# Kernel tuning notes

Measured on AMD Instinct MI355X. Metric: run time of the kernel, lower is better.

Reference implementation:

```python
import jax, jax.numpy as jnp
import numpy as np

TOTAL = 33554432  # 2**25 flat logits
NSEG = 65536      # number of jagged segments (avg len 512)


def setup_inputs() -> dict:
    key = jax.random.key(0)
    logits = jax.random.normal(key, (TOTAL,), dtype=jnp.float32)
    # Build a valid inclusive prefix-sum of segment lengths that ends exactly at TOTAL.
    rng = np.random.default_rng(0)
    raw = rng.integers(256, 769, size=NSEG).astype(np.float64)
    prefix = np.floor(np.cumsum(raw) / raw.sum() * TOTAL).astype(np.int64)
    prefix[-1] = TOTAL
    prefix_sum = jnp.asarray(prefix, dtype=jnp.int64)
    return {"logits": logits, "prefix_sum": prefix_sum}


def reference(logits, prefix_sum):
    # prefix_sum[j] = end index (exclusive) of segment j in the flat logits array.
    N = logits.shape[0]
    B = prefix_sum.shape[0]
    # segment id of element i = number of segment ends <= i
    seg = jnp.searchsorted(prefix_sum, jnp.arange(N, dtype=prefix_sum.dtype), side="right")
    # numerically stable per-segment log-softmax
    seg_max = jax.ops.segment_max(logits, seg, num_segments=B)
    seg_max = jnp.where(jnp.isfinite(seg_max), seg_max, jnp.zeros_like(seg_max))  # guard empty segments
    shifted = logits - seg_max[seg]
    seg_sum = jax.ops.segment_sum(jnp.exp(shifted), seg, num_segments=B)
    return shifted - jnp.log(seg_sum)[seg]
```

## Files before the change

### kernel.cpp

```cpp
#include <hip/hip_runtime.h>
#include <math.h>

#define WAVES_PER_BLOCK 4
#define THREADS (WAVES_PER_BLOCK * 64)
#define MAX_V4 3

__global__ __launch_bounds__(THREADS)
void jls_kernel(const float* __restrict__ logits,
                const int* __restrict__ prefix,
                float* __restrict__ out, int nseg) {
    const int wave = threadIdx.x >> 6;
    const int lane = threadIdx.x & 63;
    const int seg = blockIdx.x * WAVES_PER_BLOCK + wave;
    if (seg >= nseg) return;

    const int start = (seg == 0) ? 0 : prefix[seg - 1];
    const int end   = prefix[seg];
    const int len   = end - start;
    if (len <= 0) return;

    int a0 = (start + 3) & ~3;
    if (a0 > end) a0 = end;
    const int head = a0 - start;
    const int nv   = (end - a0) >> 2;
    const int tail_start = a0 + (nv << 2);
    const int tail = end - tail_start;

    float s = 0.f;

    if (nv <= 64 * MAX_V4) {
        float hv = 0.f, tv = 0.f;
        float4 v[MAX_V4];
        bool valid[MAX_V4];

        if (lane < head) { hv = logits[start + lane]; s += __expf(hv); }
        #pragma unroll
        for (int k = 0; k < MAX_V4; ++k) {
            const int vi = lane + k * 64;
            valid[k] = vi < nv;
            if (valid[k]) {
                v[k] = *reinterpret_cast<const float4*>(logits + a0 + (vi << 2));
                s += __expf(v[k].x) + __expf(v[k].y) + __expf(v[k].z) + __expf(v[k].w);
            }
        }
        if (lane < tail) { tv = logits[tail_start + lane]; s += __expf(tv); }

        #pragma unroll
        for (int off = 32; off > 0; off >>= 1)
            s += __shfl_xor(s, off, 64);
        const float lg = __logf(s);

        if (lane < head) out[start + lane] = hv - lg;
        #pragma unroll
        for (int k = 0; k < MAX_V4; ++k) {
            if (valid[k]) {
                const int vi = lane + k * 64;
                float4 r;
                r.x = v[k].x - lg; r.y = v[k].y - lg;
                r.z = v[k].z - lg; r.w = v[k].w - lg;
                *reinterpret_cast<float4*>(out + a0 + (vi << 2)) = r;
            }
        }
        if (lane < tail) out[tail_start + lane] = tv - lg;
    } else {
        for (int i = start + lane; i < end; i += 64)
            s += __expf(logits[i]);
        #pragma unroll
        for (int off = 32; off > 0; off >>= 1)
            s += __shfl_xor(s, off, 64);
        const float lg = __logf(s);
        for (int i = start + lane; i < end; i += 64)
            out[i] = logits[i] - lg;
    }
}

extern "C" void kernel_launch(void* const* d_in, const int* in_sizes, int n_in,
                              void* d_out, int out_size, void* d_ws, size_t ws_size,
                              hipStream_t stream) {
    const float* logits = (const float*)d_in[0];
    const int* prefix = (const int*)d_in[1];
    float* out = (float*)d_out;
    const int nseg = in_sizes[1];

    const int blocks = (nseg + WAVES_PER_BLOCK - 1) / WAVES_PER_BLOCK;
    jls_kernel<<<blocks, THREADS, 0, stream>>>(logits, prefix, out, nseg);
}
```

Baseline: 47.71 us.

## Process two segments per wave with batched loads and nontemporal stores

```diff
diff --git a/kernel.cpp b/kernel.cpp
--- a/kernel.cpp
+++ b/kernel.cpp
@@ -3,7 +3,24 @@
 
 #define WAVES_PER_BLOCK 4
 #define THREADS (WAVES_PER_BLOCK * 64)
+#define SEGS_PER_WAVE 2
 #define MAX_V4 3
+
+typedef float f32x4 __attribute__((ext_vector_type(4)));
+
+__device__ __forceinline__ void seg_generic(const float* __restrict__ logits,
+                                            float* __restrict__ out,
+                                            int start, int end, int lane) {
+    float s = 0.f;
+    for (int i = start + lane; i < end; i += 64)
+        s += __expf(logits[i]);
+    #pragma unroll
+    for (int off = 32; off > 0; off >>= 1)
+        s += __shfl_xor(s, off, 64);
+    const float lg = __logf(s);
+    for (int i = start + lane; i < end; i += 64)
+        out[i] = logits[i] - lg;
+}
 
 __global__ __launch_bounds__(THREADS)
 void jls_kernel(const float* __restrict__ logits,
@@ -11,66 +28,81 @@
                 float* __restrict__ out, int nseg) {
     const int wave = threadIdx.x >> 6;
     const int lane = threadIdx.x & 63;
-    const int seg = blockIdx.x * WAVES_PER_BLOCK + wave;
-    if (seg >= nseg) return;
+    const int seg0 = (blockIdx.x * WAVES_PER_BLOCK + wave) * SEGS_PER_WAVE;
+    if (seg0 >= nseg) return;
+    const bool has1 = (seg0 + 1) < nseg;
 
-    const int start = (seg == 0) ? 0 : prefix[seg - 1];
-    const int end   = prefix[seg];
-    const int len   = end - start;
-    if (len <= 0) return;
+    const int pA = (seg0 == 0) ? 0 : prefix[seg0 - 1];
+    const int pB = prefix[seg0];
+    const int pC = has1 ? prefix[seg0 + 1] : pB;
 
-    int a0 = (start + 3) & ~3;
-    if (a0 > end) a0 = end;
-    const int head = a0 - start;
-    const int nv   = (end - a0) >> 2;
-    const int tail_start = a0 + (nv << 2);
-    const int tail = end - tail_start;
+    int a0A = (pA + 3) & ~3; if (a0A > pB) a0A = pB;
+    const int headA = a0A - pA;
+    const int nvA   = (pB - a0A) >> 2;
+    const int tsA   = a0A + (nvA << 2);
+    const int tailA = pB - tsA;
 
-    float s = 0.f;
+    int a0B = (pB + 3) & ~3; if (a0B > pC) a0B = pC;
+    const int headB = a0B - pB;
+    const int nvB   = (pC - a0B) >> 2;
+    const int tsB   = a0B + (nvB << 2);
+    const int tailB = pC - tsB;
 
-    if (nv <= 64 * MAX_V4) {
-        float hv = 0.f, tv = 0.f;
-        float4 v[MAX_V4];
-        bool valid[MAX_V4];
+    if (nvA <= 64 * MAX_V4 && nvB <= 64 * MAX_V4) {
+        float hvA = 0.f, tvA = 0.f, hvB = 0.f, tvB = 0.f;
+        f32x4 vA[MAX_V4], vB[MAX_V4];
+        bool okA[MAX_V4], okB[MAX_V4];
 
-        if (lane < head) { hv = logits[start + lane]; s += __expf(hv); }
+        if (lane < headA) hvA = logits[pA + lane];
+        if (lane < headB) hvB = logits[pB + lane];
         #pragma unroll
         for (int k = 0; k < MAX_V4; ++k) {
             const int vi = lane + k * 64;
-            valid[k] = vi < nv;
-            if (valid[k]) {
-                v[k] = *reinterpret_cast<const float4*>(logits + a0 + (vi << 2));
-                s += __expf(v[k].x) + __expf(v[k].y) + __expf(v[k].z) + __expf(v[k].w);
+            okA[k] = vi < nvA;
+            if (okA[k]) vA[k] = *reinterpret_cast<const f32x4*>(logits + a0A + (vi << 2));
+            okB[k] = vi < nvB;
+            if (okB[k]) vB[k] = *reinterpret_cast<const f32x4*>(logits + a0B + (vi << 2));
+        }
+        if (lane < tailA) tvA = logits[tsA + lane];
+        if (lane < tailB) tvB = logits[tsB + lane];
+
+        float sA = (lane < headA) ? __expf(hvA) : 0.f;
+        float sB = (lane < headB) ? __expf(hvB) : 0.f;
+        #pragma unroll
+        for (int k = 0; k < MAX_V4; ++k) {
+            if (okA[k]) sA += __expf(vA[k].x) + __expf(vA[k].y) + __expf(vA[k].z) + __expf(vA[k].w);
+            if (okB[k]) sB += __expf(vB[k].x) + __expf(vB[k].y) + __expf(vB[k].z) + __expf(vB[k].w);
+        }
+        if (lane < tailA) sA += __expf(tvA);
+        if (lane < tailB) sB += __expf(tvB);
+
+        #pragma unroll
+        for (int off = 32; off > 0; off >>= 1) {
+            sA += __shfl_xor(sA, off, 64);
+            sB += __shfl_xor(sB, off, 64);
+        }
+        const float lgA = __logf(sA);
+        const float lgB = __logf(sB);
+
+        if (lane < headA) out[pA + lane] = hvA - lgA;
+        if (lane < headB) out[pB + lane] = hvB - lgB;
+        #pragma unroll
+        for (int k = 0; k < MAX_V4; ++k) {
+            const int vi = lane + k * 64;
+            if (okA[k]) {
+                f32x4 r = vA[k] - lgA;
+                __builtin_nontemporal_store(r, reinterpret_cast<f32x4*>(out + a0A + (vi << 2)));
+            }
+            if (okB[k]) {
+                f32x4 r = vB[k] - lgB;
+                __builtin_nontemporal_store(r, reinterpret_cast<f32x4*>(out + a0B + (vi << 2)));
             }
         }
-        if (lane < tail) { tv = logits[tail_start + lane]; s += __expf(tv); }
-
-        #pragma unroll
-        for (int off = 32; off > 0; off >>= 1)
-            s += __shfl_xor(s, off, 64);
-        const float lg = __logf(s);
-
-        if (lane < head) out[start + lane] = hv - lg;
-        #pragma unroll
-        for (int k = 0; k < MAX_V4; ++k) {
-            if (valid[k]) {
-                const int vi = lane + k * 64;
-                float4 r;
-                r.x = v[k].x - lg; r.y = v[k].y - lg;
-                r.z = v[k].z - lg; r.w = v[k].w - lg;
-                *reinterpret_cast<float4*>(out + a0 + (vi << 2)) = r;
-            }
-        }
-        if (lane < tail) out[tail_start + lane] = tv - lg;
+        if (lane < tailA) out[tsA + lane] = tvA - lgA;
+        if (lane < tailB) out[tsB + lane] = tvB - lgB;
     } else {
-        for (int i = start + lane; i < end; i += 64)
-            s += __expf(logits[i]);
-        #pragma unroll
-        for (int off = 32; off > 0; off >>= 1)
-            s += __shfl_xor(s, off, 64);
-        const float lg = __logf(s);
-        for (int i = start + lane; i < end; i += 64)
-            out[i] = logits[i] - lg;
+        seg_generic(logits, out, pA, pB, lane);
+        if (has1) seg_generic(logits, out, pB, pC, lane);
     }
 }
 
@@ -82,6 +114,7 @@
     float* out = (float*)d_out;
     const int nseg = in_sizes[1];
 
-    const int blocks = (nseg + WAVES_PER_BLOCK - 1) / WAVES_PER_BLOCK;
+    const int segs_per_block = WAVES_PER_BLOCK * SEGS_PER_WAVE;
+    const int blocks = (nseg + segs_per_block - 1) / segs_per_block;
     jls_kernel<<<blocks, THREADS, 0, stream>>>(logits, prefix, out, nseg);
 }
```

After: 48.25 us. No clear change (+1.1%).

## Use persistent waves with double-buffered segment prefetch and nontemporal stores

Applied to the files above, without the earlier changes.

```diff
diff --git a/kernel.cpp b/kernel.cpp
--- a/kernel.cpp
+++ b/kernel.cpp
@@ -1,9 +1,75 @@
 #include <hip/hip_runtime.h>
 #include <math.h>
 
-#define WAVES_PER_BLOCK 4
-#define THREADS (WAVES_PER_BLOCK * 64)
+#define WPB 4
+#define THREADS (WPB * 64)
 #define MAX_V4 3
+#define NBLOCKS 2048
+
+typedef float f32x4 __attribute__((ext_vector_type(4)));
+
+struct Seg {
+    int start, end, a0, nv, ts, head, tail;
+    float hv, tv;
+    f32x4 v0, v1, v2;
+};
+
+__device__ __forceinline__ void seg_generic(const float* __restrict__ logits,
+                                            float* __restrict__ out,
+                                            int start, int end, int lane) {
+    float s = 0.f;
+    for (int i = start + lane; i < end; i += 64)
+        s += __expf(logits[i]);
+    #pragma unroll
+    for (int off = 32; off > 0; off >>= 1)
+        s += __shfl_xor(s, off, 64);
+    const float lg = __logf(s);
+    for (int i = start + lane; i < end; i += 64)
+        out[i] = logits[i] - lg;
+}
+
+__device__ __forceinline__ void issue_data(Seg& S, int start, int end,
+                                           const float* __restrict__ logits, int lane) {
+    S.start = start; S.end = end;
+    int a0 = (start + 3) & ~3; if (a0 > end) a0 = end;
+    S.a0 = a0;
+    S.head = a0 - start;
+    const int nv = (end - a0) >> 2;
+    S.nv = nv;
+    S.ts = a0 + (nv << 2);
+    S.tail = end - S.ts;
+    S.hv = 0.f; S.tv = 0.f;
+    S.v0 = 0.f; S.v1 = 0.f; S.v2 = 0.f;
+    if (nv > 64 * MAX_V4) return;
+    if (lane < S.head) S.hv = logits[start + lane];
+    if (lane       < nv) S.v0 = *reinterpret_cast<const f32x4*>(logits + a0 + (lane << 2));
+    if (lane + 64  < nv) S.v1 = *reinterpret_cast<const f32x4*>(logits + a0 + ((lane + 64) << 2));
+    if (lane + 128 < nv) S.v2 = *reinterpret_cast<const f32x4*>(logits + a0 + ((lane + 128) << 2));
+    if (lane < S.tail) S.tv = logits[S.ts + lane];
+}
+
+__device__ __forceinline__ void finish(const Seg& S, const float* __restrict__ logits,
+                                       float* __restrict__ out, int lane) {
+    if (S.nv > 64 * MAX_V4) { seg_generic(logits, out, S.start, S.end, lane); return; }
+    const bool ok0 = lane < S.nv, ok1 = lane + 64 < S.nv, ok2 = lane + 128 < S.nv;
+    float s = (lane < S.head) ? __expf(S.hv) : 0.f;
+    if (ok0) s += __expf(S.v0.x) + __expf(S.v0.y) + __expf(S.v0.z) + __expf(S.v0.w);
+    if (ok1) s += __expf(S.v1.x) + __expf(S.v1.y) + __expf(S.v1.z) + __expf(S.v1.w);
+    if (ok2) s += __expf(S.v2.x) + __expf(S.v2.y) + __expf(S.v2.z) + __expf(S.v2.w);
+    if (lane < S.tail) s += __expf(S.tv);
+    #pragma unroll
+    for (int off = 32; off > 0; off >>= 1)
+        s += __shfl_xor(s, off, 64);
+    const float lg = __logf(s);
+    if (lane < S.head) out[S.start + lane] = S.hv - lg;
+    if (ok0) { f32x4 r = S.v0 - lg;
+        __builtin_nontemporal_store(r, reinterpret_cast<f32x4*>(out + S.a0 + (lane << 2))); }
+    if (ok1) { f32x4 r = S.v1 - lg;
+        __builtin_nontemporal_store(r, reinterpret_cast<f32x4*>(out + S.a0 + ((lane + 64) << 2))); }
+    if (ok2) { f32x4 r = S.v2 - lg;
+        __builtin_nontemporal_store(r, reinterpret_cast<f32x4*>(out + S.a0 + ((lane + 128) << 2))); }
+    if (lane < S.tail) out[S.ts + lane] = S.tv - lg;
+}
 
 __global__ __launch_bounds__(THREADS)
 void jls_kernel(const float* __restrict__ logits,
@@ -11,66 +77,38 @@
                 float* __restrict__ out, int nseg) {
     const int wave = threadIdx.x >> 6;
     const int lane = threadIdx.x & 63;
-    const int seg = blockIdx.x * WAVES_PER_BLOCK + wave;
-    if (seg >= nseg) return;
+    const int w = blockIdx.x * WPB + wave;
+    const int stride = gridDim.x * WPB;
+    if (w >= nseg) return;
+    const int nIter = (nseg - w + stride - 1) / stride;
+    const bool pf_ok = (nIter <= 64);
 
-    const int start = (seg == 0) ? 0 : prefix[seg - 1];
-    const int end   = prefix[seg];
-    const int len   = end - start;
-    if (len <= 0) return;
+    int pvS = 0, pvE = 0;
+    if (pf_ok && lane < nIter) {
+        const int sk = w + lane * stride;
+        pvS = (sk == 0) ? 0 : prefix[sk - 1];
+        pvE = prefix[sk];
+    }
 
-    int a0 = (start + 3) & ~3;
-    if (a0 > end) a0 = end;
-    const int head = a0 - start;
-    const int nv   = (end - a0) >> 2;
-    const int tail_start = a0 + (nv << 2);
-    const int tail = end - tail_start;
+    auto bounds = [&](int k, int& s0, int& s1) {
+        if (pf_ok) { s0 = __shfl(pvS, k, 64); s1 = __shfl(pvE, k, 64); }
+        else { const int sk = w + k * stride; s0 = (sk == 0) ? 0 : prefix[sk - 1]; s1 = prefix[sk]; }
+    };
 
-    float s = 0.f;
-
-    if (nv <= 64 * MAX_V4) {
-        float hv = 0.f, tv = 0.f;
-        float4 v[MAX_V4];
-        bool valid[MAX_V4];
-
-        if (lane < head) { hv = logits[start + lane]; s += __expf(hv); }
-        #pragma unroll
-        for (int k = 0; k < MAX_V4; ++k) {
-            const int vi = lane + k * 64;
-            valid[k] = vi < nv;
-            if (valid[k]) {
-                v[k] = *reinterpret_cast<const float4*>(logits + a0 + (vi << 2));
-                s += __expf(v[k].x) + __expf(v[k].y) + __expf(v[k].z) + __expf(v[k].w);
-            }
-        }
-        if (lane < tail) { tv = logits[tail_start + lane]; s += __expf(tv); }
-
-        #pragma unroll
-        for (int off = 32; off > 0; off >>= 1)
-            s += __shfl_xor(s, off, 64);
-        const float lg = __logf(s);
-
-        if (lane < head) out[start + lane] = hv - lg;
-        #pragma unroll
-        for (int k = 0; k < MAX_V4; ++k) {
-            if (valid[k]) {
-                const int vi = lane + k * 64;
-                float4 r;
-                r.x = v[k].x - lg; r.y = v[k].y - lg;
-                r.z = v[k].z - lg; r.w = v[k].w - lg;
-                *reinterpret_cast<float4*>(out + a0 + (vi << 2)) = r;
-            }
-        }
-        if (lane < tail) out[tail_start + lane] = tv - lg;
-    } else {
-        for (int i = start + lane; i < end; i += 64)
-            s += __expf(logits[i]);
-        #pragma unroll
-        for (int off = 32; off > 0; off >>= 1)
-            s += __shfl_xor(s, off, 64);
-        const float lg = __logf(s);
-        for (int i = start + lane; i < end; i += 64)
-            out[i] = logits[i] - lg;
+    Seg A, B;
+    int it = 0;
+    { int s0, s1; bounds(0, s0, s1); issue_data(A, s0, s1, logits, lane); }
+    while (true) {
+        const bool hb = (it + 1) < nIter;
+        if (hb) { int s0, s1; bounds(it + 1, s0, s1); issue_data(B, s0, s1, logits, lane); }
+        finish(A, logits, out, lane);
+        if (!hb) break;
+        ++it;
+        const bool hc = (it + 1) < nIter;
+        if (hc) { int s0, s1; bounds(it + 1, s0, s1); issue_data(A, s0, s1, logits, lane); }
+        finish(B, logits, out, lane);
+        if (!hc) break;
+        ++it;
     }
 }
 
@@ -82,6 +120,7 @@
     float* out = (float*)d_out;
     const int nseg = in_sizes[1];
 
-    const int blocks = (nseg + WAVES_PER_BLOCK - 1) / WAVES_PER_BLOCK;
+    int blocks = (nseg + WPB - 1) / WPB;
+    if (blocks > NBLOCKS) blocks = NBLOCKS;
     jls_kernel<<<blocks, THREADS, 0, stream>>>(logits, prefix, out, nseg);
 }
```

Result: no change. 48.08 us (+0.8%).
